# Performance work log

Hardware: AMD Instinct MI355X
Metric: run time of the kernel (lower is better)

Reference implementation:

```python
import jax, jax.numpy as jnp
import numpy as np

H = 512          # size_half
K = 16           # n_segments
B = 8192         # batch
WIDTH = 1.0 / K  # spline bin width


def setup_inputs() -> dict:
    key = jax.random.key(0)
    ks = jax.random.split(key, 4)
    v_in = jax.random.uniform(ks[0], (B, 2 * H), dtype=jnp.float32)  # config in [0,1]
    log_density = jax.random.normal(ks[1], (B, 1), dtype=jnp.float32)
    W1 = jax.random.normal(ks[2], (H, H), dtype=jnp.float32) * (1.0 / np.sqrt(H))
    b1 = jnp.zeros((H,), dtype=jnp.float32)
    W2 = jax.random.normal(ks[3], (H, H * K), dtype=jnp.float32) * (1.0 / np.sqrt(H))
    b2 = jnp.zeros((H * K,), dtype=jnp.float32)
    return {"v_in": v_in, "log_density": log_density, "W1": W1, "b1": b1, "W2": W2, "b2": b2}


def reference(v_in, log_density, W1, b1, W2, b2):
    # even_sites=True: passive = first half, active = second half
    v_passive = v_in[:, :H]           # [B, H]
    v_active = v_in[:, H:]            # [B, H]

    # FullyConnectedNeuralNetwork: hidden layer + final layer, tanh activation on both
    h = jnp.tanh((v_passive - 0.5) @ W1 + b1)          # [B, H]
    net = jnp.tanh(h @ W2 + b2).reshape(-1, H, K)      # [B, H, K]
    p = jax.nn.softmax(net, axis=2)                    # bin probability masses P_k

    # y-coordinates of knots: CDF of the bin masses, with leading zero
    knots_y = jnp.concatenate(
        [jnp.zeros((p.shape[0], H, 1), p.dtype), jnp.cumsum(p, axis=2)], axis=2
    )                                                  # [B, H, K+1]

    # searchsorted on uniform knots linspace(0,1,K+1), then -1, clamped
    knots_x = jnp.linspace(0.0, 1.0, K + 1, dtype=v_in.dtype)
    k = jnp.clip(jnp.searchsorted(knots_x, v_active, side="left") - 1, 0, K - 1)  # [B, H]

    p_k = jnp.take_along_axis(p, k[..., None], axis=2)[..., 0]        # [B, H]
    y_lo = jnp.take_along_axis(knots_y, k[..., None], axis=2)[..., 0]  # [B, H]

    alpha = (v_active - k.astype(v_in.dtype) * WIDTH) / WIDTH          # [B, H]
    v_out_active = y_lo + alpha * p_k

    v_out = jnp.concatenate([v_passive, v_out_active], axis=1)         # [B, 2H]
    log_density_out = log_density - jnp.sum(jnp.log(p_k), axis=1, keepdims=True)  # [B, 1]
    return v_out, log_density_out
```

## Files before the change

kernel.cpp:

```cpp
#include <hip/hip_runtime.h>
#include <hip/hip_bf16.h>

#define HH   512
#define BB   8192
#define WIDTH (1.0f/16.0f)

typedef __attribute__((ext_vector_type(8))) short  short8;
typedef __attribute__((ext_vector_type(4))) float  floatx4;

typedef const __attribute__((address_space(1))) void* gptr_t;
typedef __attribute__((address_space(3))) void*       lptr_t;

__device__ __forceinline__ void gload_lds16(const void* g, void* l) {
    __builtin_amdgcn_global_load_lds((gptr_t)g, (lptr_t)l, 16, 0, 0);
}

__device__ __forceinline__ float tanh_fast(float x) {
    float e = __expf(2.0f * x);
    return 1.0f - 2.0f * __builtin_amdgcn_rcpf(e + 1.0f);
}

__global__ void prep_all(const float* __restrict__ vin, const float* __restrict__ W1,
                         const float* __restrict__ W2, const float* __restrict__ ld,
                         float* __restrict__ vout, float* __restrict__ ldout,
                         __hip_bfloat16* __restrict__ Abf,
                         __hip_bfloat16* __restrict__ W1T,
                         __hip_bfloat16* __restrict__ W2T) {
    __shared__ float tile[32][33];
    int bid = blockIdx.x, tid = threadIdx.x;
    if (bid < 4352) {
        const float* src;  __hip_bfloat16* dst;  int cols, c0, r0;
        if (bid < 4096) { src = W2; dst = W2T; cols = 8192; c0 = (bid & 255) * 32; r0 = (bid >> 8) * 32; }
        else            { int b = bid - 4096; src = W1; dst = W1T; cols = 512; c0 = (b & 15) * 32; r0 = (b >> 4) * 32; }
        int x = tid & 31, y = tid >> 5;
        #pragma unroll
        for (int i = 0; i < 32; i += 8)
            tile[y + i][x] = src[(size_t)(r0 + y + i) * cols + c0 + x];
        __syncthreads();
        #pragma unroll
        for (int i = 0; i < 32; i += 8)
            dst[(size_t)(c0 + y + i) * 512 + r0 + x] = __float2bfloat16(tile[x][y + i]);
    } else {
        int b = bid - 4352;
        int i = b * 256 + tid;
        int r = i >> 6, c = i & 63;
        const float4* src = (const float4*)(vin + (size_t)r * 1024 + c * 8);
        float4 f0 = src[0], f1 = src[1];
        float4* dst = (float4*)(vout + (size_t)r * 1024 + c * 8);
        dst[0] = f0; dst[1] = f1;
        union { __hip_bfloat16 h[8]; uint4 v; } u;
        u.h[0] = __float2bfloat16(f0.x - 0.5f); u.h[1] = __float2bfloat16(f0.y - 0.5f);
        u.h[2] = __float2bfloat16(f0.z - 0.5f); u.h[3] = __float2bfloat16(f0.w - 0.5f);
        u.h[4] = __float2bfloat16(f1.x - 0.5f); u.h[5] = __float2bfloat16(f1.y - 0.5f);
        u.h[6] = __float2bfloat16(f1.z - 0.5f); u.h[7] = __float2bfloat16(f1.w - 0.5f);
        *(uint4*)(Abf + (size_t)r * 512 + c * 8) = u.v;
        if (tid < 4) { int row = b * 4 + tid; ldout[row] = ld[row]; }
    }
}

__global__ __launch_bounds__(256, 4) void gemm1_kernel(
        const __hip_bfloat16* __restrict__ Abf,
        const __hip_bfloat16* __restrict__ W1T,
        const float* __restrict__ b1,
        __hip_bfloat16* __restrict__ hM) {
    __shared__ short ldsA[64 * 32];
    __shared__ short ldsB[128 * 32];
    int tid = threadIdx.x;
    int lane = tid & 63;
    int wv = tid >> 6, wr = wv >> 1, wc = wv & 1;
    int q = lane >> 4, cx = lane & 15;
    int rowBase = blockIdx.y * 64;
    int colBase = blockIdx.x * 128;
    floatx4 acc[2][4] = {};

    for (int k0 = 0; k0 < HH; k0 += 32) {
        {
            int row = tid >> 2, kc = tid & 3;
            unsigned loff = __builtin_amdgcn_readfirstlane((unsigned)((tid & 192) * 16));
            gload_lds16(Abf + (size_t)(rowBase + row) * HH + k0 + kc * 8, (char*)ldsA + loff);
        }
        #pragma unroll
        for (int j = 0; j < 2; ++j) {
            int i = j * 256 + tid;
            int row = i >> 2, kc = i & 3;
            unsigned loff = __builtin_amdgcn_readfirstlane((unsigned)((j * 256 + (tid & 192)) * 16));
            gload_lds16(W1T + (size_t)(colBase + row) * HH + k0 + kc * 8, (char*)ldsB + loff);
        }
        __syncthreads();
        short8 a[2], b[4];
        #pragma unroll
        for (int mt = 0; mt < 2; ++mt)
            a[mt] = *(const short8*)(ldsA + (wr * 32 + mt * 16 + cx) * 32 + q * 8);
        #pragma unroll
        for (int nt = 0; nt < 4; ++nt)
            b[nt] = *(const short8*)(ldsB + (wc * 64 + nt * 16 + cx) * 32 + q * 8);
        #pragma unroll
        for (int mt = 0; mt < 2; ++mt)
            #pragma unroll
            for (int nt = 0; nt < 4; ++nt)
                acc[mt][nt] = __builtin_amdgcn_mfma_f32_16x16x32_bf16(a[mt], b[nt], acc[mt][nt], 0, 0, 0);
        __syncthreads();
    }

    float b1v[4];
    #pragma unroll
    for (int nt = 0; nt < 4; ++nt) b1v[nt] = b1[colBase + wc * 64 + nt * 16 + cx];
    #pragma unroll
    for (int mt = 0; mt < 2; ++mt)
        #pragma unroll
        for (int nt = 0; nt < 4; ++nt) {
            int col = colBase + wc * 64 + nt * 16 + cx;
            #pragma unroll
            for (int r = 0; r < 4; ++r) {
                int row = rowBase + wr * 32 + mt * 16 + q * 4 + r;
                hM[(size_t)row * HH + col] = __float2bfloat16(tanh_fast(acc[mt][nt][r] + b1v[nt]));
            }
        }
}

__global__ __launch_bounds__(256, 4) void gemm2_kernel(
        const __hip_bfloat16* __restrict__ hM,
        const __hip_bfloat16* __restrict__ W2T,
        const float* __restrict__ b2,
        const float* __restrict__ vin,
        float* __restrict__ vout,
        float* __restrict__ ldout) {
    __shared__ __align__(16) char smem[32768];
    short* ldsA = (short*)smem;
    short* ldsB = (short*)(smem + 16384);
    float* ldsE = (float*)smem;
    int tid = threadIdx.x;
    int lane = tid & 63;
    int wv = tid >> 6, wr = wv >> 1, wc = wv & 1;
    int q = lane >> 4, cx = lane & 15;
    int bid = blockIdx.x;
    int xcd = bid & 7, w = bid >> 3;
    int by  = xcd * 8 + (w & 7);
    int bx  = w >> 3;
    int rowBase = by * 128;
    int colBase = bx * 128;
    floatx4 acc[4][4] = {};

    for (int k0 = 0; k0 < HH; k0 += 64) {
        #pragma unroll
        for (int j = 0; j < 4; ++j) {
            int chunk = j * 256 + tid;
            int half  = j >> 1;
            int c2    = chunk & 511;
            int row = c2 >> 2, kc = c2 & 3;
            unsigned loff = __builtin_amdgcn_readfirstlane((unsigned)((j * 256 + (tid & 192)) * 16));
            gload_lds16(hM  + (size_t)(rowBase + row) * HH + k0 + half * 32 + kc * 8, (char*)ldsA + loff);
            gload_lds16(W2T + (size_t)(colBase + row) * HH + k0 + half * 32 + kc * 8, (char*)ldsB + loff);
        }
        __syncthreads();
        #pragma unroll
        for (int s = 0; s < 2; ++s) {
            const short* pA = ldsA + s * 4096;
            const short* pB = ldsB + s * 4096;
            short8 a[4], b[4];
            #pragma unroll
            for (int mt = 0; mt < 4; ++mt)
                a[mt] = *(const short8*)(pA + (wr * 64 + mt * 16 + cx) * 32 + q * 8);
            #pragma unroll
            for (int nt = 0; nt < 4; ++nt)
                b[nt] = *(const short8*)(pB + (wc * 64 + nt * 16 + cx) * 32 + q * 8);
            #pragma unroll
            for (int mt = 0; mt < 4; ++mt)
                #pragma unroll
                for (int nt = 0; nt < 4; ++nt)
                    acc[mt][nt] = __builtin_amdgcn_mfma_f32_16x16x32_bf16(a[mt], b[nt], acc[mt][nt], 0, 0, 0);
        }
        __syncthreads();
    }

    float b2v[4];
    #pragma unroll
    for (int nt = 0; nt < 4; ++nt) b2v[nt] = b2[colBase + wc * 64 + nt * 16 + cx];

    float* myTile = ldsE + wv * (16 * 68);
    int rowL  = lane & 15;
    int gL    = lane >> 4;
    int gAbs  = bx * 8 + wc * 4 + gL;

    #pragma unroll
    for (int mt = 0; mt < 4; ++mt) {
        #pragma unroll
        for (int nt = 0; nt < 4; ++nt)
            #pragma unroll
            for (int r = 0; r < 4; ++r)
                myTile[(q * 4 + r) * 68 + nt * 16 + cx] = acc[mt][nt][r] + b2v[nt];

        floatx4 x0 = *(const floatx4*)(myTile + rowL * 68 + gL * 16);
        floatx4 x1 = *(const floatx4*)(myTile + rowL * 68 + gL * 16 + 4);
        floatx4 x2 = *(const floatx4*)(myTile + rowL * 68 + gL * 16 + 8);
        floatx4 x3 = *(const floatx4*)(myTile + rowL * 68 + gL * 16 + 12);
        float xs[16] = { x0[0],x0[1],x0[2],x0[3], x1[0],x1[1],x1[2],x1[3],
                         x2[0],x2[1],x2[2],x2[3], x3[0],x3[1],x3[2],x3[3] };

        int row = rowBase + wr * 64 + mt * 16 + rowL;
        float v = vin[(size_t)row * 1024 + 512 + gAbs];
        int k = (int)ceilf(v * 16.0f) - 1;
        k = min(15, max(0, k));

        float s = 0.0f, csum = 0.0f, ek = 0.0f;
        #pragma unroll
        for (int j = 0; j < 16; ++j) {
            float e2 = __expf(2.0f * xs[j]);
            float t  = 1.0f - 2.0f * __builtin_amdgcn_rcpf(e2 + 1.0f);
            float e  = __expf(t);
            csum += (j < k)  ? e : 0.0f;
            ek    = (j == k) ? e : ek;
            s += e;
        }
        float rs = __builtin_amdgcn_rcpf(s);
        float pk  = ek * rs;
        float ylo = csum * rs;
        float alpha = (v - (float)k * WIDTH) * 16.0f;
        vout[(size_t)row * 1024 + 512 + gAbs] = ylo + alpha * pk;

        float logp = __logf(pk);
        logp += __shfl_xor(logp, 16, 64);
        logp += __shfl_xor(logp, 32, 64);
        if (lane < 16) atomicAdd(ldout + row, -logp);
    }
}

extern "C" void kernel_launch(void* const* d_in, const int* in_sizes, int n_in,
                              void* d_out, int out_size, void* d_ws, size_t ws_size,
                              hipStream_t stream) {
    const float* vin = (const float*)d_in[0];
    const float* ld  = (const float*)d_in[1];
    const float* W1  = (const float*)d_in[2];
    const float* b1  = (const float*)d_in[3];
    const float* W2  = (const float*)d_in[4];
    const float* b2  = (const float*)d_in[5];
    float* vout  = (float*)d_out;
    float* ldout = vout + (size_t)BB * 1024;

    char* ws = (char*)d_ws;
    __hip_bfloat16* Abf = (__hip_bfloat16*)(ws);
    __hip_bfloat16* W1T = (__hip_bfloat16*)(ws + 8388608);
    __hip_bfloat16* W2T = (__hip_bfloat16*)(ws + 8912896);
    __hip_bfloat16* hM  = (__hip_bfloat16*)(ws + 17301504);

    prep_all<<<6400, 256, 0, stream>>>(vin, W1, W2, ld, vout, ldout, Abf, W1T, W2T);
    gemm1_kernel<<<dim3(4, 128), 256, 0, stream>>>(Abf, W1T, b1, hM);
    gemm2_kernel<<<4096, 256, 0, stream>>>(hM, W2T, b2, vin, vout, ldout);
}
```

Before: 204.7 us.

## Enlarge gemm2 tiles to 256x256 with double-buffered, swizzled LDS prefetch

The second GEMM moves from 128x128 tiles with 4 waves to 256x256 tiles with 8 waves. Global-to-LDS loads are double-buffered so the next K slice is fetched while MFMAs run on the current one. LDS addresses use an XOR swizzle to avoid bank conflicts, and s_setprio plus barriers interleave phases across waves. This targets lower global traffic per FLOP and hidden load latency, at the cost of 128KB of LDS per block, higher register pressure from 8x4 accumulators per wave, and fewer blocks resident.

```diff
diff --git a/kernel.cpp b/kernel.cpp
--- a/kernel.cpp
+++ b/kernel.cpp
@@ -118,78 +118,120 @@
         }
 }
 
-__global__ __launch_bounds__(256, 4) void gemm2_kernel(
+__global__ __launch_bounds__(512, 2) void gemm2_kernel(
         const __hip_bfloat16* __restrict__ hM,
         const __hip_bfloat16* __restrict__ W2T,
         const float* __restrict__ b2,
         const float* __restrict__ vin,
         float* __restrict__ vout,
         float* __restrict__ ldout) {
-    __shared__ __align__(16) char smem[32768];
-    short* ldsA = (short*)smem;
-    short* ldsB = (short*)(smem + 16384);
-    float* ldsE = (float*)smem;
+    __shared__ __align__(16) char smem[131072];
     int tid = threadIdx.x;
     int lane = tid & 63;
-    int wv = tid >> 6, wr = wv >> 1, wc = wv & 1;
+    int wv = tid >> 6;
+    int wr = wv >> 2, wc = wv & 3;
     int q = lane >> 4, cx = lane & 15;
+
     int bid = blockIdx.x;
     int xcd = bid & 7, w = bid >> 3;
-    int by  = xcd * 8 + (w & 7);
-    int bx  = w >> 3;
-    int rowBase = by * 128;
-    int colBase = bx * 128;
-    floatx4 acc[4][4] = {};
-
-    for (int k0 = 0; k0 < HH; k0 += 64) {
-        #pragma unroll
-        for (int j = 0; j < 4; ++j) {
-            int chunk = j * 256 + tid;
-            int half  = j >> 1;
-            int c2    = chunk & 511;
-            int row = c2 >> 2, kc = c2 & 3;
-            unsigned loff = __builtin_amdgcn_readfirstlane((unsigned)((j * 256 + (tid & 192)) * 16));
-            gload_lds16(hM  + (size_t)(rowBase + row) * HH + k0 + half * 32 + kc * 8, (char*)ldsA + loff);
-            gload_lds16(W2T + (size_t)(colBase + row) * HH + k0 + half * 32 + kc * 8, (char*)ldsB + loff);
-        }
-        __syncthreads();
-        #pragma unroll
-        for (int s = 0; s < 2; ++s) {
-            const short* pA = ldsA + s * 4096;
-            const short* pB = ldsB + s * 4096;
+    int by = xcd * 4 + (w & 3);
+    int bx = w >> 2;
+    int rowBase = by * 256;
+    int colBase = bx * 256;
+
+    floatx4 acc[8][4] = {};
+
+    int srow = tid >> 3;
+    int skw  = ((tid & 7) ^ (srow & 7)) << 3;
+    const __hip_bfloat16* gA0 = hM  + (size_t)(rowBase +       srow) * HH + skw;
+    const __hip_bfloat16* gA1 = hM  + (size_t)(rowBase +  64 + srow) * HH + skw;
+    const __hip_bfloat16* gA2 = hM  + (size_t)(rowBase + 128 + srow) * HH + skw;
+    const __hip_bfloat16* gA3 = hM  + (size_t)(rowBase + 192 + srow) * HH + skw;
+    const __hip_bfloat16* gB0 = W2T + (size_t)(colBase +       srow) * HH + skw;
+    const __hip_bfloat16* gB1 = W2T + (size_t)(colBase +  64 + srow) * HH + skw;
+    const __hip_bfloat16* gB2 = W2T + (size_t)(colBase + 128 + srow) * HH + skw;
+    const __hip_bfloat16* gB3 = W2T + (size_t)(colBase + 192 + srow) * HH + skw;
+    unsigned l0  = (unsigned)__builtin_amdgcn_readfirstlane((tid & 448) * 16);
+    unsigned lo0 = l0;
+    unsigned lo1 = l0 + 8192;
+    unsigned lo2 = l0 + 16384;
+    unsigned lo3 = l0 + 24576;
+
+    {
+        char* A0 = smem;
+        char* B0 = smem + 65536;
+        gload_lds16(gA0, A0 + lo0); gload_lds16(gA1, A0 + lo1);
+        gload_lds16(gA2, A0 + lo2); gload_lds16(gA3, A0 + lo3);
+        gload_lds16(gB0, B0 + lo0); gload_lds16(gB1, B0 + lo1);
+        gload_lds16(gB2, B0 + lo2); gload_lds16(gB3, B0 + lo3);
+    }
+
+    for (int t = 0; t < 8; ++t) {
+        const short* Ac = (const short*)(smem + (t & 1) * 32768);
+        const short* Bc = (const short*)(smem + 65536 + (t & 1) * 32768);
+        char* An = smem + ((t & 1) ^ 1) * 32768;
+        char* Bn = smem + 65536 + ((t & 1) ^ 1) * 32768;
+        int kn = (t + 1) * 64;
+
+        asm volatile("s_waitcnt vmcnt(0)" ::: "memory");
+        __builtin_amdgcn_sched_barrier(0);
+        __builtin_amdgcn_s_barrier();
+        __builtin_amdgcn_sched_barrier(0);
+
+        #pragma unroll
+        for (int ph = 0; ph < 4; ++ph) {
+            const int kk = ph >> 1, mh = ph & 1;
             short8 a[4], b[4];
             #pragma unroll
-            for (int mt = 0; mt < 4; ++mt)
-                a[mt] = *(const short8*)(pA + (wr * 64 + mt * 16 + cx) * 32 + q * 8);
-            #pragma unroll
-            for (int nt = 0; nt < 4; ++nt)
-                b[nt] = *(const short8*)(pB + (wc * 64 + nt * 16 + cx) * 32 + q * 8);
-            #pragma unroll
-            for (int mt = 0; mt < 4; ++mt)
+            for (int i = 0; i < 4; ++i) {
+                int rowA = wr * 128 + (mh * 4 + i) * 16 + cx;
+                a[i] = *(const short8*)(Ac + rowA * 64 + (((kk * 4 + q) ^ (cx & 7)) << 3));
+            }
+            #pragma unroll
+            for (int nt = 0; nt < 4; ++nt) {
+                int rowB = wc * 64 + nt * 16 + cx;
+                b[nt] = *(const short8*)(Bc + rowB * 64 + (((kk * 4 + q) ^ (cx & 7)) << 3));
+            }
+            if (t < 7) {
+                if (ph == 0) {
+                    gload_lds16(gA0 + kn, An + lo0); gload_lds16(gA1 + kn, An + lo1);
+                    gload_lds16(gA2 + kn, An + lo2); gload_lds16(gA3 + kn, An + lo3);
+                } else if (ph == 1) {
+                    gload_lds16(gB0 + kn, Bn + lo0); gload_lds16(gB1 + kn, Bn + lo1);
+                    gload_lds16(gB2 + kn, Bn + lo2); gload_lds16(gB3 + kn, Bn + lo3);
+                }
+            }
+            __builtin_amdgcn_sched_barrier(0);
+            __builtin_amdgcn_s_barrier();
+            __builtin_amdgcn_sched_barrier(0);
+            __builtin_amdgcn_s_setprio(1);
+            #pragma unroll
+            for (int i = 0; i < 4; ++i)
                 #pragma unroll
                 for (int nt = 0; nt < 4; ++nt)
-                    acc[mt][nt] = __builtin_amdgcn_mfma_f32_16x16x32_bf16(a[mt], b[nt], acc[mt][nt], 0, 0, 0);
-        }
-        __syncthreads();
-    }
-
+                    acc[mh * 4 + i][nt] = __builtin_amdgcn_mfma_f32_16x16x32_bf16(
+                        a[i], b[nt], acc[mh * 4 + i][nt], 0, 0, 0);
+            __builtin_amdgcn_s_setprio(0);
+            __builtin_amdgcn_sched_barrier(0);
+            __builtin_amdgcn_s_barrier();
+            __builtin_amdgcn_sched_barrier(0);
+        }
+    }
+
+    float* ldsE = (float*)smem;
+    float* myTile = ldsE + wv * (16 * 68);
+    int rowL = lane & 15, gL = lane >> 4;
     float b2v[4];
     #pragma unroll
     for (int nt = 0; nt < 4; ++nt) b2v[nt] = b2[colBase + wc * 64 + nt * 16 + cx];
 
-    float* myTile = ldsE + wv * (16 * 68);
-    int rowL  = lane & 15;
-    int gL    = lane >> 4;
-    int gAbs  = bx * 8 + wc * 4 + gL;
-
-    #pragma unroll
-    for (int mt = 0; mt < 4; ++mt) {
+    #pragma unroll
+    for (int m = 0; m < 8; ++m) {
         #pragma unroll
         for (int nt = 0; nt < 4; ++nt)
             #pragma unroll
             for (int r = 0; r < 4; ++r)
-                myTile[(q * 4 + r) * 68 + nt * 16 + cx] = acc[mt][nt][r] + b2v[nt];
-
+                myTile[(q * 4 + r) * 68 + nt * 16 + cx] = acc[m][nt][r] + b2v[nt];
         floatx4 x0 = *(const floatx4*)(myTile + rowL * 68 + gL * 16);
         floatx4 x1 = *(const floatx4*)(myTile + rowL * 68 + gL * 16 + 4);
         floatx4 x2 = *(const floatx4*)(myTile + rowL * 68 + gL * 16 + 8);
@@ -197,7 +239,8 @@
         float xs[16] = { x0[0],x0[1],x0[2],x0[3], x1[0],x1[1],x1[2],x1[3],
                          x2[0],x2[1],x2[2],x2[3], x3[0],x3[1],x3[2],x3[3] };
 
-        int row = rowBase + wr * 64 + mt * 16 + rowL;
+        int row  = rowBase + wr * 128 + m * 16 + rowL;
+        int gAbs = bx * 16 + wc * 4 + gL;
         float v = vin[(size_t)row * 1024 + 512 + gAbs];
         int k = (int)ceilf(v * 16.0f) - 1;
         k = min(15, max(0, k));
@@ -206,8 +249,8 @@
         #pragma unroll
         for (int j = 0; j < 16; ++j) {
             float e2 = __expf(2.0f * xs[j]);
-            float t  = 1.0f - 2.0f * __builtin_amdgcn_rcpf(e2 + 1.0f);
-            float e  = __expf(t);
+            float tt = 1.0f - 2.0f * __builtin_amdgcn_rcpf(e2 + 1.0f);
+            float e  = __expf(tt);
             csum += (j < k)  ? e : 0.0f;
             ek    = (j == k) ? e : ek;
             s += e;
@@ -245,5 +288,5 @@
 
     prep_all<<<6400, 256, 0, stream>>>(vin, W1, W2, ld, vout, ldout, Abf, W1T, W2T);
     gemm1_kernel<<<dim3(4, 128), 256, 0, stream>>>(Abf, W1T, b1, hM);
-    gemm2_kernel<<<4096, 256, 0, stream>>>(hM, W2T, b2, vin, vout, ldout);
-}
+    gemm2_kernel<<<1024, 512, 0, stream>>>(hM, W2T, b2, vin, vout, ldout);
+}
```

Measured after the change: 212.3 us. +3.7%, slower.

## Swizzle GEMM LDS tiles with XOR layout, enlarge gemm1 tile, vectorize transpose

Applied to the files above, without the earlier changes.

Both GEMM kernels now stage A and B tiles in LDS as 64-wide K rows with an XOR swizzle on the 16-byte chunk index, so the MFMA fragment reads avoid bank conflicts. gemm1 grows its tile from 64x128 to 128x128 with K-step 64, matching the gemm2 structure and halving the grid. The weight transpose in prep_all uses float4 loads and 8-byte bf16 stores through a padded tile, and the gemm2 epilogue pads its scratch tile stride from 68 to 76. The larger gemm1 tile cuts its block count to 256, which may leave some CUs idle.

```diff
diff --git a/kernel.cpp b/kernel.cpp
--- a/kernel.cpp
+++ b/kernel.cpp
@@ -26,20 +26,25 @@
                          __hip_bfloat16* __restrict__ Abf,
                          __hip_bfloat16* __restrict__ W1T,
                          __hip_bfloat16* __restrict__ W2T) {
-    __shared__ float tile[32][33];
+    __shared__ __align__(16) float tile[32 * 36];
     int bid = blockIdx.x, tid = threadIdx.x;
     if (bid < 4352) {
         const float* src;  __hip_bfloat16* dst;  int cols, c0, r0;
         if (bid < 4096) { src = W2; dst = W2T; cols = 8192; c0 = (bid & 255) * 32; r0 = (bid >> 8) * 32; }
         else            { int b = bid - 4096; src = W1; dst = W1T; cols = 512; c0 = (b & 15) * 32; r0 = (b >> 4) * 32; }
-        int x = tid & 31, y = tid >> 5;
-        #pragma unroll
-        for (int i = 0; i < 32; i += 8)
-            tile[y + i][x] = src[(size_t)(r0 + y + i) * cols + c0 + x];
-        __syncthreads();
-        #pragma unroll
-        for (int i = 0; i < 32; i += 8)
-            dst[(size_t)(c0 + y + i) * 512 + r0 + x] = __float2bfloat16(tile[x][y + i]);
+        int y  = tid >> 3;
+        int x0 = (tid & 7) * 4;
+        float4 v = *(const float4*)(src + (size_t)(r0 + y) * cols + c0 + x0);
+        *(float4*)(tile + y * 36 + x0) = v;
+        __syncthreads();
+        int n  = tid >> 3;
+        int k4 = (tid & 7) * 4;
+        union { __hip_bfloat16 h[4]; uint2 u; } o;
+        o.h[0] = __float2bfloat16(tile[(k4 + 0) * 36 + n]);
+        o.h[1] = __float2bfloat16(tile[(k4 + 1) * 36 + n]);
+        o.h[2] = __float2bfloat16(tile[(k4 + 2) * 36 + n]);
+        o.h[3] = __float2bfloat16(tile[(k4 + 3) * 36 + n]);
+        *(uint2*)(dst + (size_t)(c0 + n) * 512 + r0 + k4) = o.u;
     } else {
         int b = bid - 4352;
         int i = b * 256 + tid;
@@ -63,42 +68,45 @@
         const __hip_bfloat16* __restrict__ W1T,
         const float* __restrict__ b1,
         __hip_bfloat16* __restrict__ hM) {
-    __shared__ short ldsA[64 * 32];
-    __shared__ short ldsB[128 * 32];
+    __shared__ __align__(16) char smem[32768];
+    short* ldsA = (short*)smem;
+    short* ldsB = (short*)(smem + 16384);
     int tid = threadIdx.x;
     int lane = tid & 63;
     int wv = tid >> 6, wr = wv >> 1, wc = wv & 1;
     int q = lane >> 4, cx = lane & 15;
-    int rowBase = blockIdx.y * 64;
+    int srow = tid >> 3;
+    int skw  = ((tid & 7) ^ (srow & 7)) * 8;
+    int rowBase = blockIdx.y * 128;
     int colBase = blockIdx.x * 128;
-    floatx4 acc[2][4] = {};
-
-    for (int k0 = 0; k0 < HH; k0 += 32) {
-        {
-            int row = tid >> 2, kc = tid & 3;
-            unsigned loff = __builtin_amdgcn_readfirstlane((unsigned)((tid & 192) * 16));
-            gload_lds16(Abf + (size_t)(rowBase + row) * HH + k0 + kc * 8, (char*)ldsA + loff);
-        }
-        #pragma unroll
-        for (int j = 0; j < 2; ++j) {
-            int i = j * 256 + tid;
-            int row = i >> 2, kc = i & 3;
+    floatx4 acc[4][4] = {};
+
+    for (int k0 = 0; k0 < HH; k0 += 64) {
+        #pragma unroll
+        for (int j = 0; j < 4; ++j) {
+            int row = j * 32 + srow;
             unsigned loff = __builtin_amdgcn_readfirstlane((unsigned)((j * 256 + (tid & 192)) * 16));
-            gload_lds16(W1T + (size_t)(colBase + row) * HH + k0 + kc * 8, (char*)ldsB + loff);
-        }
-        __syncthreads();
-        short8 a[2], b[4];
-        #pragma unroll
-        for (int mt = 0; mt < 2; ++mt)
-            a[mt] = *(const short8*)(ldsA + (wr * 32 + mt * 16 + cx) * 32 + q * 8);
-        #pragma unroll
-        for (int nt = 0; nt < 4; ++nt)
-            b[nt] = *(const short8*)(ldsB + (wc * 64 + nt * 16 + cx) * 32 + q * 8);
-        #pragma unroll
-        for (int mt = 0; mt < 2; ++mt)
+            gload_lds16(Abf + (size_t)(rowBase + row) * HH + k0 + skw, (char*)ldsA + loff);
+            gload_lds16(W1T + (size_t)(colBase + row) * HH + k0 + skw, (char*)ldsB + loff);
+        }
+        __syncthreads();
+        #pragma unroll
+        for (int s = 0; s < 2; ++s) {
+            short8 a[4], b[4];
+            #pragma unroll
+            for (int mt = 0; mt < 4; ++mt)
+                a[mt] = *(const short8*)(ldsA + (wr * 64 + mt * 16 + cx) * 64
+                                              + (((s * 4 + q) ^ (cx & 7)) << 3));
             #pragma unroll
             for (int nt = 0; nt < 4; ++nt)
-                acc[mt][nt] = __builtin_amdgcn_mfma_f32_16x16x32_bf16(a[mt], b[nt], acc[mt][nt], 0, 0, 0);
+                b[nt] = *(const short8*)(ldsB + (wc * 64 + nt * 16 + cx) * 64
+                                              + (((s * 4 + q) ^ (cx & 7)) << 3));
+            #pragma unroll
+            for (int mt = 0; mt < 4; ++mt)
+                #pragma unroll
+                for (int nt = 0; nt < 4; ++nt)
+                    acc[mt][nt] = __builtin_amdgcn_mfma_f32_16x16x32_bf16(a[mt], b[nt], acc[mt][nt], 0, 0, 0);
+        }
         __syncthreads();
     }
 
@@ -106,13 +114,13 @@
     #pragma unroll
     for (int nt = 0; nt < 4; ++nt) b1v[nt] = b1[colBase + wc * 64 + nt * 16 + cx];
     #pragma unroll
-    for (int mt = 0; mt < 2; ++mt)
+    for (int mt = 0; mt < 4; ++mt)
         #pragma unroll
         for (int nt = 0; nt < 4; ++nt) {
             int col = colBase + wc * 64 + nt * 16 + cx;
             #pragma unroll
             for (int r = 0; r < 4; ++r) {
-                int row = rowBase + wr * 32 + mt * 16 + q * 4 + r;
+                int row = rowBase + wr * 64 + mt * 16 + q * 4 + r;
                 hM[(size_t)row * HH + col] = __float2bfloat16(tanh_fast(acc[mt][nt][r] + b1v[nt]));
             }
         }
@@ -133,6 +141,8 @@
     int lane = tid & 63;
     int wv = tid >> 6, wr = wv >> 1, wc = wv & 1;
     int q = lane >> 4, cx = lane & 15;
+    int srow = tid >> 3;
+    int skw  = ((tid & 7) ^ (srow & 7)) * 8;
     int bid = blockIdx.x;
     int xcd = bid & 7, w = bid >> 3;
     int by  = xcd * 8 + (w & 7);
@@ -144,26 +154,23 @@
     for (int k0 = 0; k0 < HH; k0 += 64) {
         #pragma unroll
         for (int j = 0; j < 4; ++j) {
-            int chunk = j * 256 + tid;
-            int half  = j >> 1;
-            int c2    = chunk & 511;
-            int row = c2 >> 2, kc = c2 & 3;
+            int row = j * 32 + srow;
             unsigned loff = __builtin_amdgcn_readfirstlane((unsigned)((j * 256 + (tid & 192)) * 16));
-            gload_lds16(hM  + (size_t)(rowBase + row) * HH + k0 + half * 32 + kc * 8, (char*)ldsA + loff);
-            gload_lds16(W2T + (size_t)(colBase + row) * HH + k0 + half * 32 + kc * 8, (char*)ldsB + loff);
+            gload_lds16(hM  + (size_t)(rowBase + row) * HH + k0 + skw, (char*)ldsA + loff);
+            gload_lds16(W2T + (size_t)(colBase + row) * HH + k0 + skw, (char*)ldsB + loff);
         }
         __syncthreads();
         #pragma unroll
         for (int s = 0; s < 2; ++s) {
-            const short* pA = ldsA + s * 4096;
-            const short* pB = ldsB + s * 4096;
             short8 a[4], b[4];
             #pragma unroll
             for (int mt = 0; mt < 4; ++mt)
-                a[mt] = *(const short8*)(pA + (wr * 64 + mt * 16 + cx) * 32 + q * 8);
+                a[mt] = *(const short8*)(ldsA + (wr * 64 + mt * 16 + cx) * 64
+                                              + (((s * 4 + q) ^ (cx & 7)) << 3));
             #pragma unroll
             for (int nt = 0; nt < 4; ++nt)
-                b[nt] = *(const short8*)(pB + (wc * 64 + nt * 16 + cx) * 32 + q * 8);
+                b[nt] = *(const short8*)(ldsB + (wc * 64 + nt * 16 + cx) * 64
+                                              + (((s * 4 + q) ^ (cx & 7)) << 3));
             #pragma unroll
             for (int mt = 0; mt < 4; ++mt)
                 #pragma unroll
@@ -177,7 +184,7 @@
     #pragma unroll
     for (int nt = 0; nt < 4; ++nt) b2v[nt] = b2[colBase + wc * 64 + nt * 16 + cx];
 
-    float* myTile = ldsE + wv * (16 * 68);
+    float* myTile = ldsE + wv * (16 * 76);
     int rowL  = lane & 15;
     int gL    = lane >> 4;
     int gAbs  = bx * 8 + wc * 4 + gL;
@@ -188,12 +195,12 @@
         for (int nt = 0; nt < 4; ++nt)
             #pragma unroll
             for (int r = 0; r < 4; ++r)
-                myTile[(q * 4 + r) * 68 + nt * 16 + cx] = acc[mt][nt][r] + b2v[nt];
-
-        floatx4 x0 = *(const floatx4*)(myTile + rowL * 68 + gL * 16);
-        floatx4 x1 = *(const floatx4*)(myTile + rowL * 68 + gL * 16 + 4);
-        floatx4 x2 = *(const floatx4*)(myTile + rowL * 68 + gL * 16 + 8);
-        floatx4 x3 = *(const floatx4*)(myTile + rowL * 68 + gL * 16 + 12);
+                myTile[(q * 4 + r) * 76 + nt * 16 + cx] = acc[mt][nt][r] + b2v[nt];
+
+        floatx4 x0 = *(const floatx4*)(myTile + rowL * 76 + gL * 16);
+        floatx4 x1 = *(const floatx4*)(myTile + rowL * 76 + gL * 16 + 4);
+        floatx4 x2 = *(const floatx4*)(myTile + rowL * 76 + gL * 16 + 8);
+        floatx4 x3 = *(const floatx4*)(myTile + rowL * 76 + gL * 16 + 12);
         float xs[16] = { x0[0],x0[1],x0[2],x0[3], x1[0],x1[1],x1[2],x1[3],
                          x2[0],x2[1],x2[2],x2[3], x3[0],x3[1],x3[2],x3[3] };
 
@@ -244,6 +251,6 @@
     __hip_bfloat16* hM  = (__hip_bfloat16*)(ws + 17301504);
 
     prep_all<<<6400, 256, 0, stream>>>(vin, W1, W2, ld, vout, ldout, Abf, W1T, W2T);
-    gemm1_kernel<<<dim3(4, 128), 256, 0, stream>>>(Abf, W1T, b1, hM);
+    gemm1_kernel<<<dim3(4, 64), 256, 0, stream>>>(Abf, W1T, b1, hM);
     gemm2_kernel<<<4096, 256, 0, stream>>>(hM, W2T, b2, vin, vout, ldout);
 }
```

After: 194.3 us (median of 3 runs). 5.1% less time.
